# Kernel optimization log

Hardware: AMD Instinct MI355X
Metric: run time of the kernel (lower is better)

Reference implementation:

```python
import jax, jax.numpy as jnp
import numpy as np

HEAD_DIM = 64
D_MODEL = 512
B, T = 8, 2048


def setup_inputs() -> dict:
    key = jax.random.key(0)
    kx, kk, kq, kv = jax.random.split(key, 4)
    x = jax.random.normal(kx, (B, T, D_MODEL), dtype=jnp.float32)
    s = 1.0 / np.sqrt(D_MODEL)
    # torch nn.Linear weights are [out, in]
    Wk = jax.random.uniform(kk, (HEAD_DIM, D_MODEL), jnp.float32, -s, s)
    Wq = jax.random.uniform(kq, (HEAD_DIM, D_MODEL), jnp.float32, -s, s)
    Wv = jax.random.uniform(kv, (HEAD_DIM, D_MODEL), jnp.float32, -s, s)
    mask = jnp.ones((1,), dtype=bool)  # not-None sentinel -> causal masking on
    return {"x": x, "Wk": Wk, "Wq": Wq, "Wv": Wv, "mask": mask}


def reference(x, Wk, Wq, Wv, mask):
    Bc, Tc, C = x.shape
    k = jnp.einsum("btc,hc->bth", x, Wk)
    q = jnp.einsum("btc,hc->bth", x, Wq)
    v = jnp.einsum("btc,hc->bth", x, Wv)
    # NOTE: source scales by C**-0.5 where C == d_model (not head_dim)
    scores = jnp.einsum("bih,bjh->bij", q, k) * (C ** -0.5)  # [B,T,T]
    causal = jnp.tril(jnp.ones((Tc, Tc), dtype=bool))
    scores = jnp.where(causal[None, :, :], scores, -jnp.inf)
    # NOTE: source applies softmax over dim=1 (query axis), faithfully kept
    attn_weights = jax.nn.softmax(scores, axis=1)
    output = jnp.einsum("bij,bjh->bih", attn_weights, v)  # [B,T,head_dim]
    return (output, attn_weights)
```

## Files before the change

### kernel.cpp

```cpp
#include <hip/hip_runtime.h>
#include <hip/hip_bf16.h>

#define TT 2048
#define NB 8
#define DM 512
#define HD 64
static constexpr float SCALE = 0.04419417382415922f;

typedef short  s16x8 __attribute__((ext_vector_type(8)));
typedef float  f32x4 __attribute__((ext_vector_type(4)));

#define MFMA(a, b, c) __builtin_amdgcn_mfma_f32_16x16x32_bf16((a), (b), (c), 0, 0, 0)

static __device__ inline unsigned short f2bf(float f) {
    unsigned int u = __float_as_uint(f);
    u += 0x7FFFu + ((u >> 16) & 1u);
    return (unsigned short)(u >> 16);
}

__global__ __launch_bounds__(256) void prep_kernel(
    const float* __restrict__ Wk, const float* __restrict__ Wq,
    const float* __restrict__ Wv, unsigned short* __restrict__ wbf,
    float* __restrict__ colsum, float* __restrict__ out) {
    const int bi = blockIdx.x, t = threadIdx.x;
    const float4 z4 = make_float4(0.f, 0.f, 0.f, 0.f);
    if (bi < 1024) {
        int i = (bi * 256 + t) * 4;
        *(float4*)(out + i) = z4;
    } else if (bi < 1040) {
        int i = ((bi - 1024) * 256 + t) * 4;
        *(float4*)(colsum + i) = z4;
    } else {
        int g = ((bi - 1040) * 256 + t) * 4;
        int mat = g >> 15, off = g & 32767;
        const float* src = (mat == 0) ? Wk : (mat == 1) ? Wq : Wv;
        float4 f = *(const float4*)(src + off);
        wbf[g + 0] = f2bf(f.x); wbf[g + 1] = f2bf(f.y);
        wbf[g + 2] = f2bf(f.z); wbf[g + 3] = f2bf(f.w);
    }
}

#define XS 72
__global__ __launch_bounds__(256) void qkv_kernel(
    const float* __restrict__ x, const unsigned short* __restrict__ wbf,
    unsigned short* __restrict__ kb, unsigned short* __restrict__ qb,
    unsigned short* __restrict__ vb) {
    __shared__ unsigned short xs[32 * XS];
    const int i0 = blockIdx.x * 32;
    const int t = threadIdx.x;
    const int w = t >> 6, lane = t & 63;
    const int m15 = lane & 15, quad = lane >> 4;
    const int srow = t >> 3, c8 = (t & 7) * 8;
    f32x4 acc[2][3];
    for (int mt = 0; mt < 2; ++mt)
        for (int ct = 0; ct < 3; ++ct)
            acc[mt][ct] = (f32x4){0.f, 0.f, 0.f, 0.f};

    for (int kc = 0; kc < DM; kc += 64) {
        __syncthreads();
        {
            const float* gp = x + (size_t)(i0 + srow) * DM + kc + c8;
            float4 f0 = *(const float4*)gp;
            float4 f1 = *(const float4*)(gp + 4);
            s16x8 h;
            h[0] = (short)f2bf(f0.x); h[1] = (short)f2bf(f0.y);
            h[2] = (short)f2bf(f0.z); h[3] = (short)f2bf(f0.w);
            h[4] = (short)f2bf(f1.x); h[5] = (short)f2bf(f1.y);
            h[6] = (short)f2bf(f1.z); h[7] = (short)f2bf(f1.w);
            *(s16x8*)(xs + srow * XS + c8) = h;
        }
        __syncthreads();
        for (int ks = 0; ks < 2; ++ks) {
            s16x8 a[2];
            for (int mt = 0; mt < 2; ++mt)
                a[mt] = *(const s16x8*)(xs + (mt * 16 + m15) * XS + ks * 32 + quad * 8);
            for (int ct = 0; ct < 3; ++ct) {
                s16x8 bfr = *(const s16x8*)(wbf +
                    (size_t)((w * 3 + ct) * 16 + m15) * DM + kc + ks * 32 + quad * 8);
                acc[0][ct] = MFMA(a[0], bfr, acc[0][ct]);
                acc[1][ct] = MFMA(a[1], bfr, acc[1][ct]);
            }
        }
    }
    for (int mt = 0; mt < 2; ++mt)
        for (int ct = 0; ct < 3; ++ct) {
            int tile16 = w * 3 + ct;
            unsigned short* outp = (tile16 < 4) ? kb : (tile16 < 8) ? qb : vb;
            int col = (tile16 & 3) * 16 + m15;
            for (int r = 0; r < 4; ++r) {
                int grow = i0 + mt * 16 + quad * 4 + r;
                outp[(size_t)grow * HD + col] = f2bf(acc[mt][ct][r]);
            }
        }
}

__global__ __launch_bounds__(256) void colsum_kernel(
    const unsigned short* __restrict__ qb, const unsigned short* __restrict__ kb,
    float* __restrict__ colsum) {
    const int jt = blockIdx.x, ich = blockIdx.y, b = blockIdx.z;
    const int j0 = jt * 64;
    const int iend = (ich + 1) * 512;
    if (iend <= j0) return;
    const int t = threadIdx.x;
    const int w = t >> 6, lane = t & 63;
    const int m15 = lane & 15, quad = lane >> 4;
    s16x8 bk[4][2];
    for (int ct = 0; ct < 4; ++ct)
        for (int ks = 0; ks < 2; ++ks)
            bk[ct][ks] = *(const s16x8*)(kb +
                (size_t)(b * TT + j0 + ct * 16 + m15) * HD + ks * 32 + quad * 8);
    float csum[4] = {0.f, 0.f, 0.f, 0.f};
    const int istart = max(ich * 512, j0);
    for (int it = istart + w * 16; it < iend; it += 64) {
        s16x8 aq[2];
        for (int ks = 0; ks < 2; ++ks)
            aq[ks] = *(const s16x8*)(qb +
                (size_t)(b * TT + it + m15) * HD + ks * 32 + quad * 8);
        for (int ct = 0; ct < 4; ++ct) {
            f32x4 s = (f32x4){0.f, 0.f, 0.f, 0.f};
            s = MFMA(aq[0], bk[ct][0], s);
            s = MFMA(aq[1], bk[ct][1], s);
            int gj = j0 + ct * 16 + m15;
            for (int r = 0; r < 4; ++r) {
                int gi = it + quad * 4 + r;
                float e = (gj <= gi) ? __expf(s[r] * SCALE) : 0.f;
                csum[ct] += e;
            }
        }
    }
    for (int ct = 0; ct < 4; ++ct) {
        csum[ct] += __shfl_xor(csum[ct], 16);
        csum[ct] += __shfl_xor(csum[ct], 32);
    }
    if (lane < 16)
        for (int ct = 0; ct < 4; ++ct)
            atomicAdd(&colsum[b * TT + j0 + ct * 16 + lane], csum[ct]);
}

#define VS 136
#define PS 72
__global__ __launch_bounds__(256, 4) void normpv_kernel(
    const unsigned short* __restrict__ qb, const unsigned short* __restrict__ kb,
    const unsigned short* __restrict__ vb, const float* __restrict__ cs_g,
    float* __restrict__ attn, float* __restrict__ out) {
    const int jch = blockIdx.x;
    const int ti = blockIdx.y, b = blockIdx.z;
    const int i0 = ti * 64;
    const int jbase = jch * 512;
    float* abase = attn + (size_t)b * TT * TT;
    const int t = threadIdx.x;
    const float4 z4 = make_float4(0.f, 0.f, 0.f, 0.f);
    if (jbase > i0 + 63) {
        for (int e = 0; e < 32; ++e) {
            int f4 = e * 256 + t;
            int row = f4 >> 7, c4 = (f4 & 127) * 4;
            *(float4*)(abase + (size_t)(i0 + row) * TT + jbase + c4) = z4;
        }
        return;
    }
    const int w = t >> 6, lane = t & 63;
    const int m15 = lane & 15, quad = lane >> 4;
    __shared__ unsigned short vT[64 * VS];
    __shared__ unsigned short ps[4 * 16 * PS];
    unsigned short* psw = ps + w * 16 * PS;
    s16x8 aq[2];
    for (int ks = 0; ks < 2; ++ks)
        aq[ks] = *(const s16x8*)(qb +
            (size_t)(b * TT + i0 + w * 16 + m15) * HD + ks * 32 + quad * 8);
    f32x4 o[4];
    for (int ht = 0; ht < 4; ++ht) o[ht] = (f32x4){0.f, 0.f, 0.f, 0.f};
    const float* rcb = cs_g + b * TT;

    for (int qtr = 0; qtr < 4; ++qtr) {
        const int jh = jbase + qtr * 128;
        if (jh > i0 + 63) {
            for (int e = 0; e < 8; ++e) {
                int f4 = e * 256 + t;
                int row = f4 >> 5, c4 = (f4 & 31) * 4;
                *(float4*)(abase + (size_t)(i0 + row) * TT + jh + c4) = z4;
            }
            continue;
        }
        __syncthreads();
        {
            const int vrow = t & 127, hseg = (t >> 7) * 32;
            const unsigned short* vp =
                vb + (size_t)(b * TT + jh + vrow) * HD + hseg;
            for (int seg = 0; seg < 4; ++seg) {
                s16x8 vv = *(const s16x8*)(vp + seg * 8);
                for (int qe = 0; qe < 8; ++qe)
                    vT[(hseg + seg * 8 + qe) * VS + vrow] = (unsigned short)vv[qe];
            }
        }
        __syncthreads();
        for (int jt2 = 0; jt2 < 2; ++jt2) {
            const int j0 = jh + jt2 * 64;
            if (j0 > i0 + 63) {
                for (int e = 0; e < 4; ++e) {
                    int f4 = e * 256 + t;
                    int row = f4 >> 4, c4 = (f4 & 15) * 4;
                    *(float4*)(abase + (size_t)(i0 + row) * TT + j0 + c4) = z4;
                }
                continue;
            }
            s16x8 bk[4][2];
            for (int ct = 0; ct < 4; ++ct)
                for (int ks = 0; ks < 2; ++ks)
                    bk[ct][ks] = *(const s16x8*)(kb +
                        (size_t)(b * TT + j0 + ct * 16 + m15) * HD + ks * 32 + quad * 8);
            for (int ct = 0; ct < 4; ++ct) {
                f32x4 s = (f32x4){0.f, 0.f, 0.f, 0.f};
                s = MFMA(aq[0], bk[ct][0], s);
                s = MFMA(aq[1], bk[ct][1], s);
                int gj = j0 + ct * 16 + m15;
                float rc = __builtin_amdgcn_rcpf(rcb[gj]);
                for (int r = 0; r < 4; ++r) {
                    int gi = i0 + w * 16 + quad * 4 + r;
                    float e = (gj <= gi) ? __expf(s[r] * SCALE) : 0.f;
                    float a = e * rc;
                    abase[(size_t)gi * TT + gj] = a;
                    psw[(quad * 4 + r) * PS + ct * 16 + m15] = f2bf(a);
                }
            }
            for (int ks = 0; ks < 2; ++ks) {
                s16x8 ap = *(const s16x8*)(psw + m15 * PS + ks * 32 + quad * 8);
                for (int ht = 0; ht < 4; ++ht) {
                    s16x8 bv = *(const s16x8*)(vT +
                        (ht * 16 + m15) * VS + jt2 * 64 + ks * 32 + quad * 8);
                    o[ht] = MFMA(ap, bv, o[ht]);
                }
            }
        }
    }
    for (int ht = 0; ht < 4; ++ht)
        for (int r = 0; r < 4; ++r)
            atomicAdd(&out[(size_t)(b * TT + i0 + w * 16 + quad * 4 + r) * HD +
                           ht * 16 + m15], o[ht][r]);
}

extern "C" void kernel_launch(void* const* d_in, const int* in_sizes, int n_in,
                              void* d_out, int out_size, void* d_ws, size_t ws_size,
                              hipStream_t stream) {
    const float* x  = (const float*)d_in[0];
    const float* Wk = (const float*)d_in[1];
    const float* Wq = (const float*)d_in[2];
    const float* Wv = (const float*)d_in[3];

    float* out  = (float*)d_out;
    float* attn = out + (size_t)NB * TT * HD;

    unsigned short* kb = (unsigned short*)d_ws;
    unsigned short* qb = kb + (size_t)NB * TT * HD;
    unsigned short* vb = qb + (size_t)NB * TT * HD;
    float* colsum = (float*)(vb + (size_t)NB * TT * HD);
    unsigned short* wbf = (unsigned short*)(colsum + NB * TT);

    hipLaunchKernelGGL(prep_kernel, dim3(1136), dim3(256), 0, stream,
                       Wk, Wq, Wv, wbf, colsum, out);
    hipLaunchKernelGGL(qkv_kernel,  dim3(512), dim3(256), 0, stream,
                       x, wbf, kb, qb, vb);
    hipLaunchKernelGGL(colsum_kernel, dim3(32, 4, 8), dim3(256), 0, stream,
                       qb, kb, colsum);
    hipLaunchKernelGGL(normpv_kernel, dim3(4, 32, 8), dim3(256), 0, stream,
                       qb, kb, vb, colsum, attn, out);
}
```

Baseline: 230.9 us.

## Shrink QKV tile, double-buffer x staging with register prefetch, skip mask on full tiles

The QKV projection kernel now processes 16 rows per block instead of 32 and launches twice as many blocks. It stages x through a double-buffered shared tile with a register prefetch of the next chunk, which removes one barrier per k-step. The aim is more parallelism and overlap of global loads with MFMA work, at the cost of reloading weight fragments across twice as many blocks. In the attention kernel, tiles that sit entirely below the diagonal take a branch-free path with no causal compare.

```diff
diff --git a/kernel.cpp b/kernel.cpp
--- a/kernel.cpp
+++ b/kernel.cpp
@@ -45,53 +45,44 @@
     const float* __restrict__ x, const unsigned short* __restrict__ wbf,
     unsigned short* __restrict__ kb, unsigned short* __restrict__ qb,
     unsigned short* __restrict__ vb) {
-    __shared__ unsigned short xs[32 * XS];
-    const int i0 = blockIdx.x * 32;
+    __shared__ unsigned short xs[2][16 * XS];
+    const int i0 = blockIdx.x * 16;
     const int t = threadIdx.x;
     const int w = t >> 6, lane = t & 63;
     const int m15 = lane & 15, quad = lane >> 4;
-    const int srow = t >> 3, c8 = (t & 7) * 8;
-    f32x4 acc[2][3];
-    for (int mt = 0; mt < 2; ++mt)
-        for (int ct = 0; ct < 3; ++ct)
-            acc[mt][ct] = (f32x4){0.f, 0.f, 0.f, 0.f};
-
-    for (int kc = 0; kc < DM; kc += 64) {
-        __syncthreads();
+    const int srow = t >> 4, c4 = (t & 15) * 4;
+    const float* xrow = x + (size_t)(i0 + srow) * DM + c4;
+    f32x4 acc[3];
+    for (int ct = 0; ct < 3; ++ct) acc[ct] = (f32x4){0.f, 0.f, 0.f, 0.f};
+
+    float4 pf = *(const float4*)xrow;
+    for (int kc = 0, kci = 0; kc < DM; kc += 64, ++kci) {
         {
-            const float* gp = x + (size_t)(i0 + srow) * DM + kc + c8;
-            float4 f0 = *(const float4*)gp;
-            float4 f1 = *(const float4*)(gp + 4);
-            s16x8 h;
-            h[0] = (short)f2bf(f0.x); h[1] = (short)f2bf(f0.y);
-            h[2] = (short)f2bf(f0.z); h[3] = (short)f2bf(f0.w);
-            h[4] = (short)f2bf(f1.x); h[5] = (short)f2bf(f1.y);
-            h[6] = (short)f2bf(f1.z); h[7] = (short)f2bf(f1.w);
-            *(s16x8*)(xs + srow * XS + c8) = h;
-        }
+            ushort4 h;
+            h.x = f2bf(pf.x); h.y = f2bf(pf.y);
+            h.z = f2bf(pf.z); h.w = f2bf(pf.w);
+            *(ushort4*)(&xs[kci & 1][srow * XS + c4]) = h;
+        }
+        if (kc + 64 < DM) pf = *(const float4*)(xrow + kc + 64);
         __syncthreads();
         for (int ks = 0; ks < 2; ++ks) {
-            s16x8 a[2];
-            for (int mt = 0; mt < 2; ++mt)
-                a[mt] = *(const s16x8*)(xs + (mt * 16 + m15) * XS + ks * 32 + quad * 8);
+            s16x8 a = *(const s16x8*)(&xs[kci & 1][m15 * XS + ks * 32 + quad * 8]);
             for (int ct = 0; ct < 3; ++ct) {
                 s16x8 bfr = *(const s16x8*)(wbf +
                     (size_t)((w * 3 + ct) * 16 + m15) * DM + kc + ks * 32 + quad * 8);
-                acc[0][ct] = MFMA(a[0], bfr, acc[0][ct]);
-                acc[1][ct] = MFMA(a[1], bfr, acc[1][ct]);
-            }
-        }
-    }
-    for (int mt = 0; mt < 2; ++mt)
-        for (int ct = 0; ct < 3; ++ct) {
-            int tile16 = w * 3 + ct;
-            unsigned short* outp = (tile16 < 4) ? kb : (tile16 < 8) ? qb : vb;
-            int col = (tile16 & 3) * 16 + m15;
-            for (int r = 0; r < 4; ++r) {
-                int grow = i0 + mt * 16 + quad * 4 + r;
-                outp[(size_t)grow * HD + col] = f2bf(acc[mt][ct][r]);
-            }
-        }
+                acc[ct] = MFMA(a, bfr, acc[ct]);
+            }
+        }
+    }
+    for (int ct = 0; ct < 3; ++ct) {
+        int tile16 = w * 3 + ct;
+        unsigned short* outp = (tile16 < 4) ? kb : (tile16 < 8) ? qb : vb;
+        int col = (tile16 & 3) * 16 + m15;
+        for (int r = 0; r < 4; ++r) {
+            int grow = i0 + quad * 4 + r;
+            outp[(size_t)grow * HD + col] = f2bf(acc[ct][r]);
+        }
+    }
 }
 
 __global__ __launch_bounds__(256) void colsum_kernel(
@@ -208,18 +199,28 @@
                 for (int ks = 0; ks < 2; ++ks)
                     bk[ct][ks] = *(const s16x8*)(kb +
                         (size_t)(b * TT + j0 + ct * 16 + m15) * HD + ks * 32 + quad * 8);
+            const bool fullmask = (j0 + 63 <= i0 + w * 16);
             for (int ct = 0; ct < 4; ++ct) {
                 f32x4 s = (f32x4){0.f, 0.f, 0.f, 0.f};
                 s = MFMA(aq[0], bk[ct][0], s);
                 s = MFMA(aq[1], bk[ct][1], s);
                 int gj = j0 + ct * 16 + m15;
                 float rc = __builtin_amdgcn_rcpf(rcb[gj]);
-                for (int r = 0; r < 4; ++r) {
-                    int gi = i0 + w * 16 + quad * 4 + r;
-                    float e = (gj <= gi) ? __expf(s[r] * SCALE) : 0.f;
-                    float a = e * rc;
-                    abase[(size_t)gi * TT + gj] = a;
-                    psw[(quad * 4 + r) * PS + ct * 16 + m15] = f2bf(a);
+                if (fullmask) {
+                    for (int r = 0; r < 4; ++r) {
+                        int gi = i0 + w * 16 + quad * 4 + r;
+                        float a = __expf(s[r] * SCALE) * rc;
+                        abase[(size_t)gi * TT + gj] = a;
+                        psw[(quad * 4 + r) * PS + ct * 16 + m15] = f2bf(a);
+                    }
+                } else {
+                    for (int r = 0; r < 4; ++r) {
+                        int gi = i0 + w * 16 + quad * 4 + r;
+                        float e = (gj <= gi) ? __expf(s[r] * SCALE) : 0.f;
+                        float a = e * rc;
+                        abase[(size_t)gi * TT + gj] = a;
+                        psw[(quad * 4 + r) * PS + ct * 16 + m15] = f2bf(a);
+                    }
                 }
             }
             for (int ks = 0; ks < 2; ++ks) {
@@ -257,7 +258,7 @@
 
     hipLaunchKernelGGL(prep_kernel, dim3(1136), dim3(256), 0, stream,
                        Wk, Wq, Wv, wbf, colsum, out);
-    hipLaunchKernelGGL(qkv_kernel,  dim3(512), dim3(256), 0, stream,
+    hipLaunchKernelGGL(qkv_kernel,  dim3(1024), dim3(256), 0, stream,
                        x, wbf, kb, qb, vb);
     hipLaunchKernelGGL(colsum_kernel, dim3(32, 4, 8), dim3(256), 0, stream,
                        qb, kb, colsum);
```

Result: no change. 235.4 us (+1.9%).
